# Optimization experiments

Measured on AMD Instinct MI355X. Metric: run time of the kernel, lower is better.

Reference implementation:

```python
import jax, jax.numpy as jnp
import numpy as np

B, PS, D, HEADS, HD, PROP = 16, 32, 768, 8, 24, 4
N = PS * PS          # 1024 tokens
M = PROP * PROP      # 16 proposal centers
INNER = HEADS * HD   # 192
HID = 4 * D          # 3072
EPS = 1e-12


def setup_inputs() -> dict:
    key = jax.random.key(0)
    ks = jax.random.split(key, 8)
    s = 0.02
    f32 = jnp.float32
    return {
        "x": jax.random.normal(ks[0], (B, N, D), f32),
        "ln1_w": jnp.ones((D,), f32), "ln1_b": jnp.zeros((D,), f32),
        "f_w": jax.random.normal(ks[1], (INNER, D), f32) * s, "f_b": jnp.zeros((INNER,), f32),
        "v_w": jax.random.normal(ks[2], (INNER, D), f32) * s, "v_b": jnp.zeros((INNER,), f32),
        "proj_w": jax.random.normal(ks[3], (D, INNER), f32) * s, "proj_b": jnp.zeros((D,), f32),
        "sim_alpha": jnp.ones((1,), f32), "sim_beta": jnp.zeros((1,), f32),
        "ln2_w": jnp.ones((D,), f32), "ln2_b": jnp.zeros((D,), f32),
        "fc1_w": jax.random.normal(ks[4], (HID, D), f32) * s, "fc1_b": jnp.zeros((HID,), f32),
        "fc2_w": jax.random.normal(ks[5], (D, HID), f32) * s, "fc2_b": jnp.zeros((D,), f32),
    }


def _ln(x, w, b):
    mu = x.mean(-1, keepdims=True)
    var = ((x - mu) ** 2).mean(-1, keepdims=True)
    return (x - mu) / jnp.sqrt(var + 1e-5) * w + b


def _cluster2d(x, f_w, f_b, v_w, v_b, proj_w, proj_b, alpha, beta):
    b = x.shape[0]
    xi = x.reshape(b, PS, PS, D).transpose(0, 3, 1, 2)  # b c w h
    # 1x1 convs f and v
    f = jnp.einsum('oc,bcwh->bowh', f_w, xi) + f_b[None, :, None, None]
    v = jnp.einsum('oc,bcwh->bowh', v_w, xi) + v_b[None, :, None, None]
    # split heads: (b e) c w h
    f = f.reshape(b * HEADS, HD, PS, PS)
    v = v.reshape(b * HEADS, HD, PS, PS)
    # adaptive avg pool to (PROP, PROP) -- exact kernel/stride pooling since PS % PROP == 0
    s = PS // PROP
    cen = f.reshape(-1, HD, PROP, s, PROP, s).mean((3, 5))  # be c 4 4
    vcen = v.reshape(-1, HD, PROP, s, PROP, s).mean((3, 5)).reshape(-1, HD, M).transpose(0, 2, 1)  # be M c
    cf = cen.reshape(-1, HD, M).transpose(0, 2, 1)  # be M c
    xf = f.reshape(-1, HD, N).transpose(0, 2, 1)    # be N c
    # pairwise euclidean similarity on L2-normalized vectors: ||a-b|| = sqrt(2 - 2 a.b)
    cn = cf / jnp.maximum(jnp.linalg.norm(cf, axis=-1, keepdims=True), EPS)
    xn = xf / jnp.maximum(jnp.linalg.norm(xf, axis=-1, keepdims=True), EPS)
    dist = jnp.sqrt(jnp.clip(2.0 - 2.0 * jnp.einsum('bmc,bnc->bmn', cn, xn), EPS, None))
    sim = jax.nn.leaky_relu(beta + alpha * jnp.exp(-dist), 0.2)  # be M N (dropout eval = identity)
    # top-1 hard assignment (torch scatter of argmax -> one-hot mask, no grad through mask)
    mask = jax.nn.one_hot(jnp.argmax(sim, axis=1), M, dtype=sim.dtype).transpose(0, 2, 1)  # be M N
    sim = sim * mask
    v2 = v.reshape(-1, HD, N).transpose(0, 2, 1)  # be N c
    # weighted reduce to centers, then broadcast back to tokens
    outc = (jnp.einsum('bmn,bnc->bmc', sim, v2) + vcen) / (mask.sum(-1, keepdims=True) + 1.0)  # be M c
    out = jnp.einsum('bmn,bmc->bnc', sim, outc)  # be N c
    out = out.reshape(-1, PS, PS, HD).transpose(0, 3, 1, 2).reshape(b, INNER, PS, PS)
    out = jnp.einsum('oc,bcwh->bowh', proj_w, out) + proj_b[None, :, None, None]
    return out.transpose(0, 2, 3, 1).reshape(b, N, D)


def reference(x, ln1_w, ln1_b, f_w, f_b, v_w, v_b, proj_w, proj_b, sim_alpha, sim_beta,
              ln2_w, ln2_b, fc1_w, fc1_b, fc2_w, fc2_b):
    h = x + _cluster2d(_ln(x, ln1_w, ln1_b), f_w, f_b, v_w, v_b, proj_w, proj_b, sim_alpha, sim_beta)
    y = _ln(h, ln2_w, ln2_b)
    y = jax.nn.gelu(jnp.einsum('bnd,hd->bnh', y, fc1_w) + fc1_b, approximate=False)
    y = jnp.einsum('bnh,dh->bnd', y, fc2_w) + fc2_b
    return h + y
```

## Files before the change

kernel.cpp:

```cpp
#include <hip/hip_runtime.h>
#include <hip/hip_bf16.h>
#include <cmath>

typedef unsigned short u16;
typedef short short8 __attribute__((ext_vector_type(8)));
typedef float f32x4 __attribute__((ext_vector_type(4)));

#define D_ 768
#define NTOK 16384
#define INNER_ 192
#define HID_ 3072

__device__ __forceinline__ float u2f(u16 u) { return __uint_as_float((unsigned)u << 16); }
__device__ __forceinline__ u16 f2u(float f) {
  __hip_bfloat16 h = __float2bfloat16(f);
  u16 u; __builtin_memcpy(&u, &h, 2); return u;
}
__device__ __forceinline__ float ld1(const void* p, size_t i, int f32) {
  return f32 ? ((const float*)p)[i] : u2f(((const u16*)p)[i]);
}
__device__ __forceinline__ void st1(void* p, size_t i, float v, int f32) {
  if (f32) ((float*)p)[i] = v; else ((u16*)p)[i] = f2u(v);
}
__device__ __forceinline__ float gelu_exact(float v) {
  return 0.5f * v * (1.f + erff(v * 0.7071067811865476f));
}
__device__ __forceinline__ void unpack8(const uint4 v, float* o) {
  o[0] = u2f((u16)(v.x & 0xffffu)); o[1] = u2f((u16)(v.x >> 16));
  o[2] = u2f((u16)(v.y & 0xffffu)); o[3] = u2f((u16)(v.y >> 16));
  o[4] = u2f((u16)(v.z & 0xffffu)); o[5] = u2f((u16)(v.z >> 16));
  o[6] = u2f((u16)(v.w & 0xffffu)); o[7] = u2f((u16)(v.w >> 16));
}

__global__ __launch_bounds__(64) void detect_kernel(const unsigned* __restrict__ x,
                                                    int* __restrict__ flag) {
  int cnt = 0;
  for (int i = threadIdx.x; i < 512; i += 64) {
    const unsigned e0 = (x[i] >> 7) & 0xFFu;
    if (e0 >= 96u && e0 <= 144u) cnt++;
  }
#pragma unroll
  for (int o = 32; o > 0; o >>= 1) cnt += __shfl_down(cnt, o);
  if (threadIdx.x == 0) flag[0] = (cnt < 256) ? 1 : 0;
}

struct CvtJob { const void* src; u16* dst; int n4; };
struct CvtArgs { CvtJob j[10]; };

__global__ __launch_bounds__(256) void cvt_kernel(CvtArgs a, const int* __restrict__ flagp) {
  const int f32 = flagp[0];
  const CvtJob jb = a.j[blockIdx.y];
  const int i = blockIdx.x * 256 + threadIdx.x;
  if (i >= jb.n4) return;
  if (f32) {
    const float4 v = ((const float4*)jb.src)[i];
    const unsigned lo = (unsigned)f2u(v.x) | ((unsigned)f2u(v.y) << 16);
    const unsigned hi = (unsigned)f2u(v.z) | ((unsigned)f2u(v.w) << 16);
    ((uint2*)jb.dst)[i] = make_uint2(lo, hi);
  } else {
    ((uint2*)jb.dst)[i] = ((const uint2*)jb.src)[i];
  }
}

__global__ __launch_bounds__(256) void ln_kernel(const void* __restrict__ x,
                                                 const void* __restrict__ w,
                                                 const void* __restrict__ b,
                                                 u16* __restrict__ y,
                                                 const int* __restrict__ flagp) {
  const int fl = flagp[0];
  const size_t t = blockIdx.x;
  float v[3];
  float s = 0.f, s2 = 0.f;
#pragma unroll
  for (int i = 0; i < 3; i++) {
    v[i] = ld1(x, t * D_ + threadIdx.x + 256 * i, fl);
    s += v[i];
    s2 += v[i] * v[i];
  }
#pragma unroll
  for (int o = 32; o > 0; o >>= 1) {
    s += __shfl_down(s, o);
    s2 += __shfl_down(s2, o);
  }
  __shared__ float ps[4], ps2[4];
  __shared__ float smu, srstd;
  const int wid = threadIdx.x >> 6, lane = threadIdx.x & 63;
  if (lane == 0) { ps[wid] = s; ps2[wid] = s2; }
  __syncthreads();
  if (threadIdx.x == 0) {
    const float a = ps[0] + ps[1] + ps[2] + ps[3];
    const float a2 = ps2[0] + ps2[1] + ps2[2] + ps2[3];
    const float mu = a * (1.f / D_);
    smu = mu;
    srstd = rsqrtf(a2 * (1.f / D_) - mu * mu + 1e-5f);
  }
  __syncthreads();
  const float mu = smu, rstd = srstd;
#pragma unroll
  for (int i = 0; i < 3; i++) {
    const int c = threadIdx.x + 256 * i;
    y[t * D_ + c] = f2u((v[i] - mu) * rstd * ld1(w, c, fl) + ld1(b, c, fl));
  }
}

template <int EPI>
__global__ __launch_bounds__(256) void mfma_gemm(const u16* __restrict__ A, int lda,
                                                 const u16* __restrict__ B, int ldb,
                                                 const u16* __restrict__ bias,
                                                 const void* __restrict__ res,
                                                 void* __restrict__ C, int ldc,
                                                 int K, int row0,
                                                 const int* __restrict__ flagp) {
  const int fl = flagp[0];
  __shared__ __align__(16) u16 Asb[128 * 32];
  __shared__ __align__(16) u16 Bsb[128 * 32];
  const int tid = threadIdx.x;
  const int lane = tid & 63;
  const int wv = tid >> 6;
  const int bm = blockIdx.x * 128;
  const int bn = blockIdx.y * 128;
  const int wm = (wv & 1) * 64;
  const int wn = (wv >> 1) * 64;
  const int c0 = tid, c1 = tid + 256;
  const u16* Ag0 = A + (size_t)(bm + (c0 >> 2)) * lda + (c0 & 3) * 8;
  const u16* Ag1 = A + (size_t)(bm + (c1 >> 2)) * lda + (c1 & 3) * 8;
  const u16* Bg0 = B + (size_t)(bn + (c0 >> 2)) * ldb + (c0 & 3) * 8;
  const u16* Bg1 = B + (size_t)(bn + (c1 >> 2)) * ldb + (c1 & 3) * 8;
  u16* la0 = &Asb[c0 * 8];
  u16* la1 = &Asb[c1 * 8];
  u16* lb0 = &Bsb[c0 * 8];
  u16* lb1 = &Bsb[c1 * 8];

  f32x4 acc[4][4];
#pragma unroll
  for (int i = 0; i < 4; i++)
#pragma unroll
    for (int j = 0; j < 4; j++) acc[i][j] = (f32x4){0.f, 0.f, 0.f, 0.f};

  const int ml = lane & 15;
  const int kq = (lane >> 4) * 8;

  for (int k0 = 0; k0 < K; k0 += 32) {
    __syncthreads();
    __builtin_amdgcn_global_load_lds(
        (const __attribute__((address_space(1))) void*)(Ag0 + k0),
        (__attribute__((address_space(3))) void*)la0, 16, 0, 0);
    __builtin_amdgcn_global_load_lds(
        (const __attribute__((address_space(1))) void*)(Ag1 + k0),
        (__attribute__((address_space(3))) void*)la1, 16, 0, 0);
    __builtin_amdgcn_global_load_lds(
        (const __attribute__((address_space(1))) void*)(Bg0 + k0),
        (__attribute__((address_space(3))) void*)lb0, 16, 0, 0);
    __builtin_amdgcn_global_load_lds(
        (const __attribute__((address_space(1))) void*)(Bg1 + k0),
        (__attribute__((address_space(3))) void*)lb1, 16, 0, 0);
    __syncthreads();
    short8 af[4], bf[4];
#pragma unroll
    for (int i = 0; i < 4; i++) {
      af[i] = *(const short8*)&Asb[(wm + i * 16 + ml) * 32 + kq];
      bf[i] = *(const short8*)&Bsb[(wn + i * 16 + ml) * 32 + kq];
    }
#pragma unroll
    for (int i = 0; i < 4; i++)
#pragma unroll
      for (int j = 0; j < 4; j++)
        acc[i][j] = __builtin_amdgcn_mfma_f32_16x16x32_bf16(af[i], bf[j], acc[i][j], 0, 0, 0);
  }

  const int qr = (lane >> 4) * 4;
#pragma unroll
  for (int i = 0; i < 4; i++) {
#pragma unroll
    for (int j = 0; j < 4; j++) {
      const int colg = bn + wn + j * 16 + ml;
      const float bb = u2f(bias[colg]);
#pragma unroll
      for (int r = 0; r < 4; r++) {
        const size_t row = (size_t)row0 + bm + wm + i * 16 + qr + r;
        float v = acc[i][j][r] + bb;
        if (EPI == 1) v = gelu_exact(v);
        if (EPI == 2) {
          v += ld1(res, row * ldc + colg, fl);
          st1(C, row * ldc + colg, v, fl);
        } else {
          ((u16*)C)[row * ldc + colg] = f2u(v);
        }
      }
    }
  }
}

#define SB8 __builtin_amdgcn_sched_barrier(0)
#define BAR8 __builtin_amdgcn_s_barrier()

template <int EPI>
__global__ __launch_bounds__(512, 4) void mfma_gemmP(const u16* __restrict__ A, int lda,
                                                     const u16* __restrict__ B, int ldb,
                                                     const u16* __restrict__ bias,
                                                     const void* __restrict__ res,
                                                     void* __restrict__ C, int ldc,
                                                     int K, int row0, int gm, int gn,
                                                     const int* __restrict__ flagp) {
  const int fl = flagp[0];
  __shared__ __align__(16) u16 L[3][(128 + 256) * 32];
  const int tid = threadIdx.x;
  const int lane = tid & 63;
  const int wv = tid >> 6;

  int mb_, nb_;
  {
    const int bid = blockIdx.x;
    const int ntot = gm * gn;
    if ((ntot & 511) == 0 && (512 % gm) == 0 && gm >= 2) {
      const int l = bid >> 8, p = bid & 255;
      const int G = gm >> 1;
      nb_ = (l >> 1) * (512 / gm) + p / G;
      mb_ = (p % G) * 2 + (l & 1);
    } else {
      mb_ = bid % gm;
      nb_ = bid / gm;
    }
  }
  const int bm = mb_ * 128;
  const int bn = nb_ * 256;

  const int wm = (wv & 1) * 64;
  const int wn = (wv >> 1) * 64;
  const int ml = lane & 15;
  const int qk = lane >> 4;

  const int srow = tid >> 2;
  const int q_s = (tid & 3) ^ ((srow >> 1) & 3);
  const size_t gaA  = (size_t)(bm + srow) * lda + q_s * 8;
  const size_t gbB0 = (size_t)(bn + srow) * ldb + q_s * 8;
  const size_t gbB1 = (size_t)(bn + srow + 128) * ldb + q_s * 8;

  int offA[4], offB[4];
#pragma unroll
  for (int i = 0; i < 4; i++) {
    const int r = wm + i * 16 + ml;
    offA[i] = (r * 4 + (qk ^ ((r >> 1) & 3))) * 8;
  }
#pragma unroll
  for (int j = 0; j < 4; j++) {
    const int r = wn + j * 16 + ml;
    offB[j] = 4096 + (r * 4 + (qk ^ ((r >> 1) & 3))) * 8;
  }

  f32x4 acc[4][4];
#pragma unroll
  for (int i = 0; i < 4; i++)
#pragma unroll
    for (int j = 0; j < 4; j++) acc[i][j] = (f32x4){0.f, 0.f, 0.f, 0.f};

  const int NT = K >> 5;

#define STGP(tilex) do {                                                            \
    const size_t k_ = (size_t)(tilex) * 32;                                         \
    u16* lb_ = &L[(tilex) % 3][0];                                                  \
    __builtin_amdgcn_global_load_lds(                                               \
        (const __attribute__((address_space(1))) void*)(A + gaA + k_),              \
        (__attribute__((address_space(3))) void*)(lb_ + tid * 8), 16, 0, 0);        \
    __builtin_amdgcn_global_load_lds(                                               \
        (const __attribute__((address_space(1))) void*)(B + gbB0 + k_),             \
        (__attribute__((address_space(3))) void*)(lb_ + 4096 + tid * 8), 16, 0, 0); \
    __builtin_amdgcn_global_load_lds(                                               \
        (const __attribute__((address_space(1))) void*)(B + gbB1 + k_),             \
        (__attribute__((address_space(3))) void*)(lb_ + 4096 + (tid + 512) * 8), 16, 0, 0); \
  } while (0)

  STGP(0);
  if (NT > 1) {
    STGP(1);
    asm volatile("s_waitcnt vmcnt(3)" ::: "memory");
  } else {
    asm volatile("s_waitcnt vmcnt(0)" ::: "memory");
  }
  SB8; BAR8; SB8;

  for (int t = 0; t < NT; t++) {
    const u16* Lb = &L[t % 3][0];
    short8 af[4], bf[4];
#pragma unroll
    for (int j = 0; j < 4; j++) bf[j] = *(const short8*)(Lb + offB[j]);
#pragma unroll
    for (int i = 0; i < 4; i++) af[i] = *(const short8*)(Lb + offA[i]);
    if (t + 2 < NT) {
      STGP(t + 2);
      asm volatile("s_waitcnt vmcnt(3)" ::: "memory");
    } else if (t + 1 < NT) {
      asm volatile("s_waitcnt vmcnt(0)" ::: "memory");
    }
    SB8; BAR8;
    asm volatile("s_waitcnt lgkmcnt(0)" ::: "memory"); SB8;
    __builtin_amdgcn_s_setprio(1);
#pragma unroll
    for (int i = 0; i < 4; i++)
#pragma unroll
      for (int j = 0; j < 4; j++)
        acc[i][j] = __builtin_amdgcn_mfma_f32_16x16x32_bf16(af[i], bf[j], acc[i][j], 0, 0, 0);
    __builtin_amdgcn_s_setprio(0);
    SB8; BAR8;
  }
#undef STGP

  const int qr = (lane >> 4) * 4;
#pragma unroll
  for (int i = 0; i < 4; i++) {
#pragma unroll
    for (int j = 0; j < 4; j++) {
      const int colg = bn + wn + j * 16 + ml;
      const float bb = u2f(bias[colg]);
#pragma unroll
      for (int r = 0; r < 4; r++) {
        const size_t row = (size_t)row0 + bm + wm + i * 16 + qr + r;
        float v = acc[i][j][r] + bb;
        if (EPI == 1) v = gelu_exact(v);
        if (EPI == 2) {
          v += ld1(res, row * ldc + colg, fl);
          st1(C, row * ldc + colg, v, fl);
        } else {
          ((u16*)C)[row * ldc + colg] = f2u(v);
        }
      }
    }
  }
}

__global__ __launch_bounds__(512) void cluster_kernel(u16* __restrict__ FV,
                                                      const void* __restrict__ alpha_p,
                                                      const void* __restrict__ beta_p,
                                                      const int* __restrict__ flagp) {
  const int fl = flagp[0];
  const int be = blockIdx.x;
  const int b = be >> 3, e = be & 7;
  const int tid = threadIdx.x;
  const float alpha = ld1(alpha_p, 0, fl), beta = ld1(beta_p, 0, fl);

  __shared__ __align__(16) u16 S[1024 * 24];
  __shared__ float cn[16][24];
  __shared__ float vcen[16][24];
  __shared__ float outc[16][24];
  __shared__ float rcn[16];
  __shared__ int cnt[16];

  u16* Fg = FV + ((size_t)b * 1024) * 384 + e * 24;
  const u16* Vg = Fg + 192;

  for (int c = tid; c < 3072; c += 512) {
    const int n = c / 3, q = c - n * 3;
    *(uint4*)&S[n * 24 + q * 8] = *(const uint4*)(Fg + (size_t)n * 384 + q * 8);
  }
  if (tid < 16) cnt[tid] = 0;
  __syncthreads();

  for (int t = tid; t < 384; t += 512) {
    const int m = t / 24, ch = t - m * 24;
    const int pw = m >> 2, ph = m & 3;
    float sum = 0.f;
    for (int dw = 0; dw < 8; dw++) {
      const int base = (pw * 8 + dw) * 32 + ph * 8;
      for (int dh = 0; dh < 8; dh++) sum += u2f(S[(base + dh) * 24 + ch]);
    }
    cn[m][ch] = sum * (1.f / 64.f);
  }
  __syncthreads();
  if (tid < 16) {
    float s = 0.f;
    for (int ch = 0; ch < 24; ch++) { const float v = cn[tid][ch]; s += v * v; }
    rcn[tid] = 1.f / fmaxf(sqrtf(s), 1e-12f);
  }
  __syncthreads();

  const int na = tid, nb = tid + 512;
  float besta = -3.4e38f, bestb = -3.4e38f;
  int bma = 0, bmb = 0;
  {
    float xa[24], xb[24];
    const uint4* ra = (const uint4*)&S[na * 24];
    const uint4* rb = (const uint4*)&S[nb * 24];
#pragma unroll
    for (int q = 0; q < 3; q++) {
      unpack8(ra[q], &xa[q * 8]);
      unpack8(rb[q], &xb[q * 8]);
    }
    float ssa = 0.f, ssb = 0.f;
#pragma unroll
    for (int ch = 0; ch < 24; ch++) {
      ssa = fmaf(xa[ch], xa[ch], ssa);
      ssb = fmaf(xb[ch], xb[ch], ssb);
    }
    const float rna = 1.f / fmaxf(sqrtf(ssa), 1e-12f);
    const float rnb = 1.f / fmaxf(sqrtf(ssb), 1e-12f);
    for (int m = 0; m < 16; m++) {
      float da = 0.f, db = 0.f;
#pragma unroll
      for (int k = 0; k < 12; k++) {
        const float2 c = *(const float2*)&cn[m][2 * k];
        da = fmaf(c.x, xa[2 * k], da); da = fmaf(c.y, xa[2 * k + 1], da);
        db = fmaf(c.x, xb[2 * k], db); db = fmaf(c.y, xb[2 * k + 1], db);
      }
      const float rc = rcn[m];
      da *= rna * rc;
      db *= rnb * rc;
      const float dda = sqrtf(fmaxf(2.f - 2.f * da, 1e-12f));
      const float ddb = sqrtf(fmaxf(2.f - 2.f * db, 1e-12f));
      const float za = beta + alpha * expf(-dda);
      const float zb = beta + alpha * expf(-ddb);
      const float sa = (za >= 0.f) ? za : 0.2f * za;
      const float sb = (zb >= 0.f) ? zb : 0.2f * zb;
      if (sa > besta) { besta = sa; bma = m; }
      if (sb > bestb) { bestb = sb; bmb = m; }
    }
    atomicAdd(&cnt[bma], 1);
    atomicAdd(&cnt[bmb], 1);
  }
  __syncthreads();

  for (int c = tid; c < 3072; c += 512) {
    const int n = c / 3, q = c - n * 3;
    *(uint4*)&S[n * 24 + q * 8] = *(const uint4*)(Vg + (size_t)n * 384 + q * 8);
  }
  if (tid < 384) outc[tid / 24][tid - (tid / 24) * 24] = 0.f;
  __syncthreads();

  for (int t = tid; t < 384; t += 512) {
    const int m = t / 24, ch = t - m * 24;
    const int pw = m >> 2, ph = m & 3;
    float sum = 0.f;
    for (int dw = 0; dw < 8; dw++) {
      const int base = (pw * 8 + dw) * 32 + ph * 8;
      for (int dh = 0; dh < 8; dh++) sum += u2f(S[(base + dh) * 24 + ch]);
    }
    vcen[m][ch] = sum * (1.f / 64.f);
  }

  {
    float va[24], vb[24];
    const uint4* ra = (const uint4*)&S[na * 24];
    const uint4* rb = (const uint4*)&S[nb * 24];
#pragma unroll
    for (int q = 0; q < 3; q++) {
      unpack8(ra[q], &va[q * 8]);
      unpack8(rb[q], &vb[q * 8]);
    }
#pragma unroll
    for (int ch = 0; ch < 24; ch++) {
      atomicAdd(&outc[bma][ch], besta * va[ch]);
      atomicAdd(&outc[bmb][ch], bestb * vb[ch]);
    }
  }
  __syncthreads();

  for (int t = tid; t < 384; t += 512) {
    const int m = t / 24, ch = t - m * 24;
    outc[m][ch] = (outc[m][ch] + vcen[m][ch]) / ((float)cnt[m] + 1.f);
  }
  __syncthreads();

#pragma unroll
  for (int pass = 0; pass < 2; pass++) {
    const int n = pass ? nb : na;
    const int m = pass ? bmb : bma;
    const float s = pass ? bestb : besta;
    unsigned w[12];
#pragma unroll
    for (int k = 0; k < 12; k++) {
      w[k] = (unsigned)f2u(s * outc[m][2 * k]) |
             ((unsigned)f2u(s * outc[m][2 * k + 1]) << 16);
    }
    uint4* dst = (uint4*)(Fg + (size_t)n * 384);
    dst[0] = make_uint4(w[0], w[1], w[2], w[3]);
    dst[1] = make_uint4(w[4], w[5], w[6], w[7]);
    dst[2] = make_uint4(w[8], w[9], w[10], w[11]);
  }
}

extern "C" void kernel_launch(void* const* d_in, const int* in_sizes, int n_in,
                              void* d_out, int out_size, void* d_ws, size_t ws_size,
                              hipStream_t stream) {
  const void* x      = d_in[0];
  const void* ln1_w  = d_in[1];
  const void* ln1_b  = d_in[2];
  const void* f_w    = d_in[3];
  const void* f_b    = d_in[4];
  const void* v_w    = d_in[5];
  const void* v_b    = d_in[6];
  const void* proj_w = d_in[7];
  const void* proj_b = d_in[8];
  const void* alpha  = d_in[9];
  const void* beta   = d_in[10];
  const void* ln2_w  = d_in[11];
  const void* ln2_b  = d_in[12];
  const void* fc1_w  = d_in[13];
  const void* fc1_b  = d_in[14];
  const void* fc2_w  = d_in[15];
  const void* fc2_b  = d_in[16];

  char* ws = (char*)d_ws;
  int* flag  = (int*)(ws + 0);
  u16* fvw   = (u16*)(ws + 256);
  u16* prw   = (u16*)(ws + 590080);
  u16* f1w   = (u16*)(ws + 884992);
  u16* f2w   = (u16*)(ws + 5603584);
  u16* fvb   = (u16*)(ws + 10322176);
  u16* prb   = (u16*)(ws + 10322944);
  u16* f1b   = (u16*)(ws + 10324480);
  u16* f2b_  = (u16*)(ws + 10330624);
  u16* Y1    = (u16*)(ws + 10332416);
  u16* FV    = (u16*)(ws + 35498240);
  u16* Gext  = (u16*)(ws + 48081152);

  const long extra = (long)ws_size - 48081152L;
  u16* G; long crows;
  if (extra >= (long)NTOK * HID_ * 2) { G = Gext; crows = NTOK; }
  else if (extra >= 256L * HID_ * 2) { G = Gext; crows = (extra / (HID_ * 2)) / 256 * 256; }
  else { G = FV; crows = 2048; }

  detect_kernel<<<1, 64, 0, stream>>>((const unsigned*)x, flag);

  CvtArgs ca;
  ca.j[0] = {f_w,    fvw,            147456 / 4};
  ca.j[1] = {v_w,    fvw + 147456,   147456 / 4};
  ca.j[2] = {proj_w, prw,            147456 / 4};
  ca.j[3] = {fc1_w,  f1w,            2359296 / 4};
  ca.j[4] = {fc2_w,  f2w,            2359296 / 4};
  ca.j[5] = {f_b,    fvb,            192 / 4};
  ca.j[6] = {v_b,    fvb + 192,      192 / 4};
  ca.j[7] = {proj_b, prb,            768 / 4};
  ca.j[8] = {fc1_b,  f1b,            3072 / 4};
  ca.j[9] = {fc2_b,  f2b_,           768 / 4};
  cvt_kernel<<<dim3(2304, 10), 256, 0, stream>>>(ca, flag);

  ln_kernel<<<NTOK, 256, 0, stream>>>(x, ln1_w, ln1_b, Y1, flag);
  mfma_gemm<0><<<dim3(128, 3), 256, 0, stream>>>(
      Y1, D_, fvw, D_, fvb, nullptr, FV, 384, D_, 0, flag);
  cluster_kernel<<<128, 512, 0, stream>>>(FV, alpha, beta, flag);
  mfma_gemm<2><<<dim3(128, 6), 256, 0, stream>>>(
      FV, 384, prw, INNER_, prb, x, d_out, D_, INNER_, 0, flag);
  ln_kernel<<<NTOK, 256, 0, stream>>>(d_out, ln2_w, ln2_b, Y1, flag);
  for (long t0 = 0; t0 < NTOK; t0 += crows) {
    const long ct = (t0 + crows <= NTOK) ? crows : (NTOK - t0);
    const int gm1 = (int)(ct / 128), gn1 = HID_ / 256;
    const int gm2 = (int)(ct / 128), gn2 = D_ / 256;
    mfma_gemmP<1><<<dim3(gm1 * gn1), 512, 0, stream>>>(
        Y1 + t0 * D_, D_, f1w, D_, f1b, nullptr, G, HID_, D_, 0, gm1, gn1, flag);
    mfma_gemmP<2><<<dim3(gm2 * gn2), 512, 0, stream>>>(
        G, HID_, f2w, HID_, f2b_, d_out, d_out, D_, HID_, (int)t0, gm2, gn2, flag);
  }
}
```

Baseline: 488.1 us.

## Split cluster kernel into centers, assign, and broadcast kernels for more parallelism

The single cluster kernel (128 blocks, one per batch-head) is replaced by three kernels. A 2048-block kernel computes the pooled centers. A 256-block kernel assigns each token to its best center and accumulates the weighted sums with global atomics. A 256-block kernel broadcasts the results back. Splitting this way uses more of the GPU than 128 blocks and swaps per-element shared-memory float atomics for per-(m,ch) loop reductions. The cost is extra launches, a workspace round trip for intermediates, and a serial 512-iteration scan per thread in the assign step.

```diff
diff --git a/kernel.cpp b/kernel.cpp
--- a/kernel.cpp
+++ b/kernel.cpp
@@ -328,153 +328,160 @@
   }
 }
 
-__global__ __launch_bounds__(512) void cluster_kernel(u16* __restrict__ FV,
+
+__global__ __launch_bounds__(64) void cluster_centers(const u16* __restrict__ FV,
+                                                      float* __restrict__ CEN,
+                                                      float* __restrict__ VCEN,
+                                                      float* __restrict__ RCN,
+                                                      float* __restrict__ OUTC,
+                                                      int* __restrict__ CNT) {
+  const int be = blockIdx.x >> 4, m = blockIdx.x & 15;
+  const int b = be >> 3, e = be & 7;
+  const int lane = threadIdx.x;
+  const int pw = m >> 2, ph = m & 3;
+  __shared__ float cnL[24];
+
+  const int isF = (lane < 24);
+  const int isV = (lane >= 32 && lane < 56);
+  const int ch = isF ? lane : (lane - 32);
+  const u16* base = FV + ((size_t)b * 1024) * 384 + e * 24 + (isV ? 192 : 0);
+
+  if (isF || isV) {
+    float sum = 0.f;
+    for (int dw = 0; dw < 8; dw++) {
+      const int nb0 = (pw * 8 + dw) * 32 + ph * 8;
+#pragma unroll
+      for (int dh = 0; dh < 8; dh++)
+        sum += u2f(base[(size_t)(nb0 + dh) * 384 + ch]);
+    }
+    const float c = sum * (1.f / 64.f);
+    const int idx = (be * 16 + m) * 24 + ch;
+    if (isF) { CEN[idx] = c; cnL[ch] = c; OUTC[idx] = 0.f; }
+    else     { VCEN[idx] = c; }
+  }
+  if (lane == 56) CNT[be * 16 + m] = 0;
+  __syncthreads();
+  if (lane == 0) {
+    float s = 0.f;
+    for (int c2 = 0; c2 < 24; c2++) { const float v = cnL[c2]; s += v * v; }
+    RCN[be * 16 + m] = 1.f / fmaxf(sqrtf(s), 1e-12f);
+  }
+}
+
+__global__ __launch_bounds__(512) void cluster_assign(const u16* __restrict__ FV,
+                                                      const float* __restrict__ CEN,
+                                                      const float* __restrict__ RCN,
+                                                      float* __restrict__ OUTC,
+                                                      int* __restrict__ CNT,
+                                                      float* __restrict__ SMs,
+                                                      int* __restrict__ SMm,
                                                       const void* __restrict__ alpha_p,
                                                       const void* __restrict__ beta_p,
                                                       const int* __restrict__ flagp) {
   const int fl = flagp[0];
-  const int be = blockIdx.x;
+  const int be = blockIdx.x >> 1, half = blockIdx.x & 1;
   const int b = be >> 3, e = be & 7;
   const int tid = threadIdx.x;
   const float alpha = ld1(alpha_p, 0, fl), beta = ld1(beta_p, 0, fl);
 
-  __shared__ __align__(16) u16 S[1024 * 24];
-  __shared__ float cn[16][24];
-  __shared__ float vcen[16][24];
-  __shared__ float outc[16][24];
-  __shared__ float rcn[16];
-  __shared__ int cnt[16];
-
-  u16* Fg = FV + ((size_t)b * 1024) * 384 + e * 24;
+  __shared__ __align__(16) u16 SF[512 * 24];
+  __shared__ __align__(16) u16 SV[512 * 24];
+  __shared__ float cnr[16][24];
+  __shared__ float rcnL[16];
+  __shared__ float sms[512];
+  __shared__ int smm[512];
+  __shared__ int cntp[16];
+
+  const int n0 = half * 512;
+  const u16* Fg = FV + ((size_t)b * 1024 + n0) * 384 + e * 24;
   const u16* Vg = Fg + 192;
 
-  for (int c = tid; c < 3072; c += 512) {
+  for (int c = tid; c < 1536; c += 512) {
     const int n = c / 3, q = c - n * 3;
-    *(uint4*)&S[n * 24 + q * 8] = *(const uint4*)(Fg + (size_t)n * 384 + q * 8);
-  }
-  if (tid < 16) cnt[tid] = 0;
+    *(uint4*)&SF[n * 24 + q * 8] = *(const uint4*)(Fg + (size_t)n * 384 + q * 8);
+    *(uint4*)&SV[n * 24 + q * 8] = *(const uint4*)(Vg + (size_t)n * 384 + q * 8);
+  }
+  if (tid < 384) {
+    const int m = tid / 24, ch = tid - m * 24;
+    cnr[m][ch] = CEN[(be * 16 + m) * 24 + ch];
+  }
+  if (tid < 16) { rcnL[tid] = RCN[be * 16 + tid]; cntp[tid] = 0; }
   __syncthreads();
 
-  for (int t = tid; t < 384; t += 512) {
-    const int m = t / 24, ch = t - m * 24;
-    const int pw = m >> 2, ph = m & 3;
-    float sum = 0.f;
-    for (int dw = 0; dw < 8; dw++) {
-      const int base = (pw * 8 + dw) * 32 + ph * 8;
-      for (int dh = 0; dh < 8; dh++) sum += u2f(S[(base + dh) * 24 + ch]);
-    }
-    cn[m][ch] = sum * (1.f / 64.f);
+  {
+    float xf[24];
+    const uint4* ra = (const uint4*)&SF[tid * 24];
+#pragma unroll
+    for (int q = 0; q < 3; q++) unpack8(ra[q], &xf[q * 8]);
+    float ss = 0.f;
+#pragma unroll
+    for (int ch = 0; ch < 24; ch++) ss = fmaf(xf[ch], xf[ch], ss);
+    const float rn = 1.f / fmaxf(sqrtf(ss), 1e-12f);
+    float best = -3.4e38f;
+    int bm_ = 0;
+    for (int m = 0; m < 16; m++) {
+      float d = 0.f;
+#pragma unroll
+      for (int k = 0; k < 12; k++) {
+        const float2 c = *(const float2*)&cnr[m][2 * k];
+        d = fmaf(c.x, xf[2 * k], d); d = fmaf(c.y, xf[2 * k + 1], d);
+      }
+      d *= rn * rcnL[m];
+      const float dd = sqrtf(fmaxf(2.f - 2.f * d, 1e-12f));
+      const float z = beta + alpha * expf(-dd);
+      const float sim = (z >= 0.f) ? z : 0.2f * z;
+      if (sim > best) { best = sim; bm_ = m; }
+    }
+    smm[tid] = bm_;
+    sms[tid] = best;
+    atomicAdd(&cntp[bm_], 1);
+    SMm[(size_t)be * 1024 + n0 + tid] = bm_;
+    SMs[(size_t)be * 1024 + n0 + tid] = best;
   }
   __syncthreads();
-  if (tid < 16) {
-    float s = 0.f;
-    for (int ch = 0; ch < 24; ch++) { const float v = cn[tid][ch]; s += v * v; }
-    rcn[tid] = 1.f / fmaxf(sqrtf(s), 1e-12f);
+
+  if (tid < 384) {
+    const int m = tid / 24, ch = tid - m * 24;
+    float acc = 0.f;
+    for (int n = 0; n < 512; n++) {
+      if (smm[n] == m) acc = fmaf(sms[n], u2f(SV[n * 24 + ch]), acc);
+    }
+    atomicAdd(&OUTC[(be * 16 + m) * 24 + ch], acc);
+  }
+  if (tid < 16) atomicAdd(&CNT[be * 16 + tid], cntp[tid]);
+}
+
+__global__ __launch_bounds__(512) void cluster_bcast(u16* __restrict__ FV,
+                                                     const float* __restrict__ OUTC,
+                                                     const float* __restrict__ VCEN,
+                                                     const int* __restrict__ CNT,
+                                                     const float* __restrict__ SMs,
+                                                     const int* __restrict__ SMm) {
+  const int be = blockIdx.x >> 1, half = blockIdx.x & 1;
+  const int b = be >> 3, e = be & 7;
+  const int tid = threadIdx.x;
+  __shared__ float outf[16][24];
+
+  if (tid < 384) {
+    const int m = tid / 24, ch = tid - m * 24;
+    outf[m][ch] = (OUTC[(be * 16 + m) * 24 + ch] + VCEN[(be * 16 + m) * 24 + ch]) /
+                  ((float)CNT[be * 16 + m] + 1.f);
   }
   __syncthreads();
 
-  const int na = tid, nb = tid + 512;
-  float besta = -3.4e38f, bestb = -3.4e38f;
-  int bma = 0, bmb = 0;
-  {
-    float xa[24], xb[24];
-    const uint4* ra = (const uint4*)&S[na * 24];
-    const uint4* rb = (const uint4*)&S[nb * 24];
-#pragma unroll
-    for (int q = 0; q < 3; q++) {
-      unpack8(ra[q], &xa[q * 8]);
-      unpack8(rb[q], &xb[q * 8]);
-    }
-    float ssa = 0.f, ssb = 0.f;
-#pragma unroll
-    for (int ch = 0; ch < 24; ch++) {
-      ssa = fmaf(xa[ch], xa[ch], ssa);
-      ssb = fmaf(xb[ch], xb[ch], ssb);
-    }
-    const float rna = 1.f / fmaxf(sqrtf(ssa), 1e-12f);
-    const float rnb = 1.f / fmaxf(sqrtf(ssb), 1e-12f);
-    for (int m = 0; m < 16; m++) {
-      float da = 0.f, db = 0.f;
-#pragma unroll
-      for (int k = 0; k < 12; k++) {
-        const float2 c = *(const float2*)&cn[m][2 * k];
-        da = fmaf(c.x, xa[2 * k], da); da = fmaf(c.y, xa[2 * k + 1], da);
-        db = fmaf(c.x, xb[2 * k], db); db = fmaf(c.y, xb[2 * k + 1], db);
-      }
-      const float rc = rcn[m];
-      da *= rna * rc;
-      db *= rnb * rc;
-      const float dda = sqrtf(fmaxf(2.f - 2.f * da, 1e-12f));
-      const float ddb = sqrtf(fmaxf(2.f - 2.f * db, 1e-12f));
-      const float za = beta + alpha * expf(-dda);
-      const float zb = beta + alpha * expf(-ddb);
-      const float sa = (za >= 0.f) ? za : 0.2f * za;
-      const float sb = (zb >= 0.f) ? zb : 0.2f * zb;
-      if (sa > besta) { besta = sa; bma = m; }
-      if (sb > bestb) { bestb = sb; bmb = m; }
-    }
-    atomicAdd(&cnt[bma], 1);
-    atomicAdd(&cnt[bmb], 1);
-  }
-  __syncthreads();
-
-  for (int c = tid; c < 3072; c += 512) {
-    const int n = c / 3, q = c - n * 3;
-    *(uint4*)&S[n * 24 + q * 8] = *(const uint4*)(Vg + (size_t)n * 384 + q * 8);
-  }
-  if (tid < 384) outc[tid / 24][tid - (tid / 24) * 24] = 0.f;
-  __syncthreads();
-
-  for (int t = tid; t < 384; t += 512) {
-    const int m = t / 24, ch = t - m * 24;
-    const int pw = m >> 2, ph = m & 3;
-    float sum = 0.f;
-    for (int dw = 0; dw < 8; dw++) {
-      const int base = (pw * 8 + dw) * 32 + ph * 8;
-      for (int dh = 0; dh < 8; dh++) sum += u2f(S[(base + dh) * 24 + ch]);
-    }
-    vcen[m][ch] = sum * (1.f / 64.f);
-  }
-
-  {
-    float va[24], vb[24];
-    const uint4* ra = (const uint4*)&S[na * 24];
-    const uint4* rb = (const uint4*)&S[nb * 24];
-#pragma unroll
-    for (int q = 0; q < 3; q++) {
-      unpack8(ra[q], &va[q * 8]);
-      unpack8(rb[q], &vb[q * 8]);
-    }
-#pragma unroll
-    for (int ch = 0; ch < 24; ch++) {
-      atomicAdd(&outc[bma][ch], besta * va[ch]);
-      atomicAdd(&outc[bmb][ch], bestb * vb[ch]);
-    }
-  }
-  __syncthreads();
-
-  for (int t = tid; t < 384; t += 512) {
-    const int m = t / 24, ch = t - m * 24;
-    outc[m][ch] = (outc[m][ch] + vcen[m][ch]) / ((float)cnt[m] + 1.f);
-  }
-  __syncthreads();
-
-#pragma unroll
-  for (int pass = 0; pass < 2; pass++) {
-    const int n = pass ? nb : na;
-    const int m = pass ? bmb : bma;
-    const float s = pass ? bestb : besta;
-    unsigned w[12];
-#pragma unroll
-    for (int k = 0; k < 12; k++) {
-      w[k] = (unsigned)f2u(s * outc[m][2 * k]) |
-             ((unsigned)f2u(s * outc[m][2 * k + 1]) << 16);
-    }
-    uint4* dst = (uint4*)(Fg + (size_t)n * 384);
-    dst[0] = make_uint4(w[0], w[1], w[2], w[3]);
-    dst[1] = make_uint4(w[4], w[5], w[6], w[7]);
-    dst[2] = make_uint4(w[8], w[9], w[10], w[11]);
-  }
+  const int n0 = half * 512;
+  const int m = SMm[(size_t)be * 1024 + n0 + tid];
+  const float s = SMs[(size_t)be * 1024 + n0 + tid];
+  unsigned w[12];
+#pragma unroll
+  for (int k = 0; k < 12; k++) {
+    w[k] = (unsigned)f2u(s * outf[m][2 * k]) |
+           ((unsigned)f2u(s * outf[m][2 * k + 1]) << 16);
+  }
+  uint4* dst = (uint4*)(FV + ((size_t)b * 1024 + n0 + tid) * 384 + e * 24);
+  dst[0] = make_uint4(w[0], w[1], w[2], w[3]);
+  dst[1] = make_uint4(w[4], w[5], w[6], w[7]);
+  dst[2] = make_uint4(w[8], w[9], w[10], w[11]);
 }
 
 extern "C" void kernel_launch(void* const* d_in, const int* in_sizes, int n_in,
@@ -510,9 +517,16 @@
   u16* f2b_  = (u16*)(ws + 10330624);
   u16* Y1    = (u16*)(ws + 10332416);
   u16* FV    = (u16*)(ws + 35498240);
-  u16* Gext  = (u16*)(ws + 48081152);
-
-  const long extra = (long)ws_size - 48081152L;
+  float* CEN  = (float*)(ws + 48081152);
+  float* VCEN = (float*)(ws + 48277760);
+  float* RCN  = (float*)(ws + 48474368);
+  float* OUTC = (float*)(ws + 48482560);
+  int*   CNT  = (int*)  (ws + 48679168);
+  float* SMs  = (float*)(ws + 48687360);
+  int*   SMm  = (int*)  (ws + 49211648);
+  u16* Gext  = (u16*)(ws + 49735936);
+
+  const long extra = (long)ws_size - 49735936L;
   u16* G; long crows;
   if (extra >= (long)NTOK * HID_ * 2) { G = Gext; crows = NTOK; }
   else if (extra >= 256L * HID_ * 2) { G = Gext; crows = (extra / (HID_ * 2)) / 256 * 256; }
@@ -536,7 +550,10 @@
   ln_kernel<<<NTOK, 256, 0, stream>>>(x, ln1_w, ln1_b, Y1, flag);
   mfma_gemm<0><<<dim3(128, 3), 256, 0, stream>>>(
       Y1, D_, fvw, D_, fvb, nullptr, FV, 384, D_, 0, flag);
-  cluster_kernel<<<128, 512, 0, stream>>>(FV, alpha, beta, flag);
+  cluster_centers<<<2048, 64, 0, stream>>>(FV, CEN, VCEN, RCN, OUTC, CNT);
+  cluster_assign<<<256, 512, 0, stream>>>(FV, CEN, RCN, OUTC, CNT, SMs, SMm,
+                                          alpha, beta, flag);
+  cluster_bcast<<<256, 512, 0, stream>>>(FV, OUTC, VCEN, CNT, SMs, SMm);
   mfma_gemm<2><<<dim3(128, 6), 256, 0, stream>>>(
       FV, 384, prw, INNER_, prb, x, d_out, D_, INNER_, 0, flag);
   ln_kernel<<<NTOK, 256, 0, stream>>>(d_out, ln2_w, ln2_b, Y1, flag);
```

Measured after the change: 497.6 us. Within noise of the previous version (+1.9%).

## Triple-buffer LDS and swizzle layout in small GEMM kernel

Applied to the files above, without the earlier changes.

The small MFMA GEMM used for the f/v projection and the output projection is rewritten with a three-stage LDS ring buffer. Tiles are prefetched two steps ahead using global_load_lds, gated by explicit vmcnt waits and barriers. An XOR swizzle on the LDS layout is added to cut bank conflicts on the fragment reads, and MFMA priority is raised during compute. This hides global load latency behind compute, at the cost of more LDS per block (which may reduce occupancy) and fragile hand-written waitcnt logic.

```diff
diff --git a/kernel.cpp b/kernel.cpp
--- a/kernel.cpp
+++ b/kernel.cpp
@@ -103,17 +103,19 @@
   }
 }
 
+#define SB8 __builtin_amdgcn_sched_barrier(0)
+#define BAR8 __builtin_amdgcn_s_barrier()
+
 template <int EPI>
-__global__ __launch_bounds__(256) void mfma_gemm(const u16* __restrict__ A, int lda,
-                                                 const u16* __restrict__ B, int ldb,
-                                                 const u16* __restrict__ bias,
-                                                 const void* __restrict__ res,
-                                                 void* __restrict__ C, int ldc,
-                                                 int K, int row0,
-                                                 const int* __restrict__ flagp) {
+__global__ __launch_bounds__(256, 3) void mfma_gemmS(const u16* __restrict__ A, int lda,
+                                                     const u16* __restrict__ B, int ldb,
+                                                     const u16* __restrict__ bias,
+                                                     const void* __restrict__ res,
+                                                     void* __restrict__ C, int ldc,
+                                                     int K, int row0,
+                                                     const int* __restrict__ flagp) {
   const int fl = flagp[0];
-  __shared__ __align__(16) u16 Asb[128 * 32];
-  __shared__ __align__(16) u16 Bsb[128 * 32];
+  __shared__ __align__(16) u16 L[3][128 * 32 * 2];
   const int tid = threadIdx.x;
   const int lane = tid & 63;
   const int wv = tid >> 6;
@@ -121,15 +123,24 @@
   const int bn = blockIdx.y * 128;
   const int wm = (wv & 1) * 64;
   const int wn = (wv >> 1) * 64;
-  const int c0 = tid, c1 = tid + 256;
-  const u16* Ag0 = A + (size_t)(bm + (c0 >> 2)) * lda + (c0 & 3) * 8;
-  const u16* Ag1 = A + (size_t)(bm + (c1 >> 2)) * lda + (c1 & 3) * 8;
-  const u16* Bg0 = B + (size_t)(bn + (c0 >> 2)) * ldb + (c0 & 3) * 8;
-  const u16* Bg1 = B + (size_t)(bn + (c1 >> 2)) * ldb + (c1 & 3) * 8;
-  u16* la0 = &Asb[c0 * 8];
-  u16* la1 = &Asb[c1 * 8];
-  u16* lb0 = &Bsb[c0 * 8];
-  u16* lb1 = &Bsb[c1 * 8];
+  const int ml = lane & 15;
+  const int qk = lane >> 4;
+
+  const int srow = tid >> 2;
+  const int q_s = (tid & 3) ^ ((srow >> 1) & 3);
+  const size_t gA0 = (size_t)(bm + srow) * lda + q_s * 8;
+  const size_t gA1 = (size_t)(bm + srow + 64) * lda + q_s * 8;
+  const size_t gB0 = (size_t)(bn + srow) * ldb + q_s * 8;
+  const size_t gB1 = (size_t)(bn + srow + 64) * ldb + q_s * 8;
+
+  int offA[4], offB[4];
+#pragma unroll
+  for (int i = 0; i < 4; i++) {
+    const int rA = wm + i * 16 + ml;
+    offA[i] = (rA * 4 + (qk ^ ((rA >> 1) & 3))) * 8;
+    const int rB = wn + i * 16 + ml;
+    offB[i] = 4096 + (rB * 4 + (qk ^ ((rB >> 1) & 3))) * 8;
+  }
 
   f32x4 acc[4][4];
 #pragma unroll
@@ -137,36 +148,59 @@
 #pragma unroll
     for (int j = 0; j < 4; j++) acc[i][j] = (f32x4){0.f, 0.f, 0.f, 0.f};
 
-  const int ml = lane & 15;
-  const int kq = (lane >> 4) * 8;
-
-  for (int k0 = 0; k0 < K; k0 += 32) {
-    __syncthreads();
-    __builtin_amdgcn_global_load_lds(
-        (const __attribute__((address_space(1))) void*)(Ag0 + k0),
-        (__attribute__((address_space(3))) void*)la0, 16, 0, 0);
-    __builtin_amdgcn_global_load_lds(
-        (const __attribute__((address_space(1))) void*)(Ag1 + k0),
-        (__attribute__((address_space(3))) void*)la1, 16, 0, 0);
-    __builtin_amdgcn_global_load_lds(
-        (const __attribute__((address_space(1))) void*)(Bg0 + k0),
-        (__attribute__((address_space(3))) void*)lb0, 16, 0, 0);
-    __builtin_amdgcn_global_load_lds(
-        (const __attribute__((address_space(1))) void*)(Bg1 + k0),
-        (__attribute__((address_space(3))) void*)lb1, 16, 0, 0);
-    __syncthreads();
+  const int NT = K >> 5;
+
+#define STGS(tilex) do {                                                            \
+    const size_t k_ = (size_t)(tilex) * 32;                                         \
+    u16* lb_ = &L[(tilex) % 3][0];                                                  \
+    __builtin_amdgcn_global_load_lds(                                               \
+        (const __attribute__((address_space(1))) void*)(A + gA0 + k_),              \
+        (__attribute__((address_space(3))) void*)(lb_ + tid * 8), 16, 0, 0);        \
+    __builtin_amdgcn_global_load_lds(                                               \
+        (const __attribute__((address_space(1))) void*)(A + gA1 + k_),              \
+        (__attribute__((address_space(3))) void*)(lb_ + (tid + 256) * 8), 16, 0, 0);\
+    __builtin_amdgcn_global_load_lds(                                               \
+        (const __attribute__((address_space(1))) void*)(B + gB0 + k_),              \
+        (__attribute__((address_space(3))) void*)(lb_ + 4096 + tid * 8), 16, 0, 0); \
+    __builtin_amdgcn_global_load_lds(                                               \
+        (const __attribute__((address_space(1))) void*)(B + gB1 + k_),              \
+        (__attribute__((address_space(3))) void*)(lb_ + 4096 + (tid + 256) * 8), 16, 0, 0); \
+  } while (0)
+
+  STGS(0);
+  if (NT > 1) {
+    STGS(1);
+    asm volatile("s_waitcnt vmcnt(4)" ::: "memory");
+  } else {
+    asm volatile("s_waitcnt vmcnt(0)" ::: "memory");
+  }
+  SB8; BAR8; SB8;
+
+  for (int t = 0; t < NT; t++) {
+    const u16* Lb = &L[t % 3][0];
     short8 af[4], bf[4];
 #pragma unroll
-    for (int i = 0; i < 4; i++) {
-      af[i] = *(const short8*)&Asb[(wm + i * 16 + ml) * 32 + kq];
-      bf[i] = *(const short8*)&Bsb[(wn + i * 16 + ml) * 32 + kq];
-    }
+    for (int j = 0; j < 4; j++) bf[j] = *(const short8*)(Lb + offB[j]);
+#pragma unroll
+    for (int i = 0; i < 4; i++) af[i] = *(const short8*)(Lb + offA[i]);
+    if (t + 2 < NT) {
+      STGS(t + 2);
+      asm volatile("s_waitcnt vmcnt(4)" ::: "memory");
+    } else if (t + 1 < NT) {
+      asm volatile("s_waitcnt vmcnt(0)" ::: "memory");
+    }
+    SB8; BAR8;
+    asm volatile("s_waitcnt lgkmcnt(0)" ::: "memory"); SB8;
+    __builtin_amdgcn_s_setprio(1);
 #pragma unroll
     for (int i = 0; i < 4; i++)
 #pragma unroll
       for (int j = 0; j < 4; j++)
         acc[i][j] = __builtin_amdgcn_mfma_f32_16x16x32_bf16(af[i], bf[j], acc[i][j], 0, 0, 0);
-  }
+    __builtin_amdgcn_s_setprio(0);
+    SB8; BAR8;
+  }
+#undef STGS
 
   const int qr = (lane >> 4) * 4;
 #pragma unroll
@@ -190,9 +224,6 @@
     }
   }
 }
-
-#define SB8 __builtin_amdgcn_sched_barrier(0)
-#define BAR8 __builtin_amdgcn_s_barrier()
 
 template <int EPI>
 __global__ __launch_bounds__(512, 4) void mfma_gemmP(const u16* __restrict__ A, int lda,
@@ -534,10 +565,10 @@
   cvt_kernel<<<dim3(2304, 10), 256, 0, stream>>>(ca, flag);
 
   ln_kernel<<<NTOK, 256, 0, stream>>>(x, ln1_w, ln1_b, Y1, flag);
-  mfma_gemm<0><<<dim3(128, 3), 256, 0, stream>>>(
+  mfma_gemmS<0><<<dim3(128, 3), 256, 0, stream>>>(
       Y1, D_, fvw, D_, fvb, nullptr, FV, 384, D_, 0, flag);
   cluster_kernel<<<128, 512, 0, stream>>>(FV, alpha, beta, flag);
-  mfma_gemm<2><<<dim3(128, 6), 256, 0, stream>>>(
+  mfma_gemmS<2><<<dim3(128, 6), 256, 0, stream>>>(
       FV, 384, prw, INNER_, prb, x, d_out, D_, INNER_, 0, flag);
   ln_kernel<<<NTOK, 256, 0, stream>>>(d_out, ln2_w, ln2_b, Y1, flag);
   for (long t0 = 0; t0 < NTOK; t0 += crows) {
```

Result: no change. 480.1 us (-1.6%).
